# Performance work log

Hardware: AMD Instinct MI355X
Metric: run time of the kernel (lower is better)

The kernel has to match this reference:

```python
import jax, jax.numpy as jnp
import numpy as np

H = 8          # num_heads
D = 32         # out_feats per head
E = 500_000    # number of metapath instances (edges)
N = 100_000    # number of destination nodes
NEG_SLOPE = 0.01


def setup_inputs() -> dict:
    key = jax.random.key(0)
    k1, k2, k3 = jax.random.split(key, 3)
    feat0 = jax.random.normal(k1, (E, H * D), dtype=jnp.float32)
    # learned parameter attn_r [1, H, D] (xavier_normal in torch; plain normal suffices)
    attn_r = jax.random.normal(k2, (1, H, D), dtype=jnp.float32) * 0.1
    dst_idx = jax.random.randint(k3, (E,), 0, N)
    return {"feat0": feat0, "attn_r": attn_r, "dst_idx": dst_idx, "num_dst": N}


def reference(feat0, attn_r, dst_idx, num_dst):
    # [E, H, D] per-head metapath-instance features (feat_drop is identity in eval)
    h = feat0.reshape(-1, H, D)
    # er = sum(h * attn_r) over feature dim -> [E, H]
    er = jnp.sum(h * attn_r, axis=-1)
    # leaky relu on edge scores
    e = jnp.where(er > 0, er, NEG_SLOPE * er)
    # per-destination-node edge softmax (stable: subtract segment max)
    emax = jax.lax.stop_gradient(
        jax.ops.segment_max(e, dst_idx, num_segments=num_dst))  # [N, H]
    num = jnp.exp(e - emax[dst_idx])                            # [E, H]
    den = jax.ops.segment_sum(num, dst_idx, num_segments=num_dst)  # [N, H]
    a = num / den[dst_idx]                                      # [E, H]
    # attention-weighted scatter-sum aggregation: sum_e a_e * h_e per dst node
    m = h * a[..., None]                                        # [E, H, D]
    out = jax.ops.segment_sum(m, dst_idx, num_segments=num_dst)  # [N, H, D]
    # ELU activation then flatten heads
    out = jnp.where(out > 0, out, jnp.expm1(out))
    return out.reshape(num_dst, H * D)
```

## Files before the change

kernel.cpp:

```cpp
#include <hip/hip_runtime.h>
#include <hip/hip_bf16.h>

#define H 8
#define D 32
#define HD 256
#define NEG_SLOPE 0.01f

typedef float f32x4 __attribute__((ext_vector_type(4)));


__global__ void hist_kernel(const int* __restrict__ dst, int E, int* __restrict__ count) {
    int i = blockIdx.x * blockDim.x + threadIdx.x;
    int base = i * 4;
    if (base + 3 < E) {
        int4 d = *reinterpret_cast<const int4*>(dst + base);
        atomicAdd(&count[d.x], 1);
        atomicAdd(&count[d.y], 1);
        atomicAdd(&count[d.z], 1);
        atomicAdd(&count[d.w], 1);
    } else {
        for (int k = base; k < E; ++k) atomicAdd(&count[dst[k]], 1);
    }
}

__global__ void scan_block_kernel(const int* __restrict__ in, int n,
                                  int* __restrict__ out_excl, int* __restrict__ bsum) {
    __shared__ int s[256];
    int t = threadIdx.x;
    int i = blockIdx.x * 256 + t;
    int v = (i < n) ? in[i] : 0;
    s[t] = v;
    __syncthreads();
    for (int off = 1; off < 256; off <<= 1) {
        int x = (t >= off) ? s[t - off] : 0;
        __syncthreads();
        s[t] += x;
        __syncthreads();
    }
    if (i < n) out_excl[i] = s[t] - v;
    if (t == 255) bsum[blockIdx.x] = s[255];
}

__global__ void scan_single_kernel(int* __restrict__ data, int n) {
    __shared__ int s[1024];
    int t = threadIdx.x;
    int v = (t < n) ? data[t] : 0;
    s[t] = v;
    __syncthreads();
    for (int off = 1; off < 1024; off <<= 1) {
        int x = (t >= off) ? s[t - off] : 0;
        __syncthreads();
        s[t] += x;
        __syncthreads();
    }
    if (t < n) data[t] = s[t] - v;
}

__global__ void add_base_kernel(int* __restrict__ off, const int* __restrict__ bsum,
                                int n, int* __restrict__ cursor) {
    int i = blockIdx.x * blockDim.x + threadIdx.x;
    if (i < n) {
        int o = off[i] + bsum[i >> 8];
        off[i] = o;
        cursor[i] = o;
    }
}

__global__ void scatter_kernel(const int* __restrict__ dst, int E,
                               int* __restrict__ cursor, int* __restrict__ csr) {
    int i = blockIdx.x * blockDim.x + threadIdx.x;
    int base = i * 4;
    if (base + 3 < E) {
        int4 d = *reinterpret_cast<const int4*>(dst + base);
        int p0 = atomicAdd(&cursor[d.x], 1); csr[p0] = base;
        int p1 = atomicAdd(&cursor[d.y], 1); csr[p1] = base + 1;
        int p2 = atomicAdd(&cursor[d.z], 1); csr[p2] = base + 2;
        int p3 = atomicAdd(&cursor[d.w], 1); csr[p3] = base + 3;
    } else {
        for (int k = base; k < E; ++k) {
            int p = atomicAdd(&cursor[dst[k]], 1);
            csr[p] = k;
        }
    }
}

__global__ void aggregate_kernel(const float* __restrict__ feat,
                                 const float* __restrict__ attn_r,
                                 const int* __restrict__ csr,
                                 const int* __restrict__ offsets,
                                 const int* __restrict__ count,
                                 float* __restrict__ out, int N) {
    int gtid = blockIdx.x * blockDim.x + threadIdx.x;
    int node = gtid >> 6;
    int lane = threadIdx.x & 63;
    if (node >= N) return;

    f32x4 ar = reinterpret_cast<const f32x4*>(attn_r)[lane];
    int start = offsets[node];
    int len   = count[node];

    f32x4 acc = (f32x4)(0.f);
    float den = 0.f;

    const f32x4* featv = reinterpret_cast<const f32x4*>(feat);

    for (int base = 0; base < len; base += 64) {
        int rem = min(64, len - base);
        int iclamp = min(lane, rem - 1);
        int eidx   = csr[start + base + iclamp];

        int e0 = __shfl(eidx, 0);
        f32x4 f0 = __builtin_nontemporal_load(&featv[(size_t)e0 * 64 + lane]);
        f32x4 f1 = f0, f2 = f0, f3 = f0;
        if (rem > 1) { int e = __shfl(eidx, 1); f1 = __builtin_nontemporal_load(&featv[(size_t)e * 64 + lane]); }
        if (rem > 2) { int e = __shfl(eidx, 2); f2 = __builtin_nontemporal_load(&featv[(size_t)e * 64 + lane]); }
        if (rem > 3) { int e = __shfl(eidx, 3); f3 = __builtin_nontemporal_load(&featv[(size_t)e * 64 + lane]); }

        for (int k = 0; k < rem; ++k) {
            f32x4 f = f0;
            f0 = f1; f1 = f2; f2 = f3;
            int kn = k + 4;
            if (kn < rem) {
                int en = __shfl(eidx, kn);
                f3 = __builtin_nontemporal_load(&featv[(size_t)en * 64 + lane]);
            }
            float part = f.x * ar.x + f.y * ar.y + f.z * ar.z + f.w * ar.w;
            part += __shfl_xor(part, 1);
            part += __shfl_xor(part, 2);
            part += __shfl_xor(part, 4);
            float er  = part;
            float el  = (er > 0.f) ? er : NEG_SLOPE * er;
            float num = __expf(el);
            den   += num;
            acc.x += num * f.x;
            acc.y += num * f.y;
            acc.z += num * f.z;
            acc.w += num * f.w;
        }
    }

    float inv = (len > 0) ? (1.0f / den) : 0.0f;
    f32x4 o;
    o.x = acc.x * inv;
    o.y = acc.y * inv;
    o.z = acc.z * inv;
    o.w = acc.w * inv;
    o.x = (o.x > 0.f) ? o.x : expm1f(o.x);
    o.y = (o.y > 0.f) ? o.y : expm1f(o.y);
    o.z = (o.z > 0.f) ? o.z : expm1f(o.z);
    o.w = (o.w > 0.f) ? o.w : expm1f(o.w);
    __builtin_nontemporal_store(o, &reinterpret_cast<f32x4*>(out)[(size_t)node * 64 + lane]);
}


extern "C" void kernel_launch(void* const* d_in, const int* in_sizes, int n_in,
                              void* d_out, int out_size, void* d_ws, size_t ws_size,
                              hipStream_t stream) {
    const float* feat   = (const float*)d_in[0];
    const float* attn_r = (const float*)d_in[1];
    const int*   dst    = (const int*)d_in[2];
    float*       out    = (float*)d_out;

    const int E = in_sizes[0] / HD;
    const int N = out_size / HD;
    const int NB = (N + 255) / 256;

    int* count   = (int*)d_ws;
    int* offsets = count + N;
    int* cursor  = offsets + N;
    int* bsum    = cursor + N;
    int* csr     = bsum + 1024;

    (void)hipMemsetAsync(count, 0, (size_t)N * sizeof(int), stream);

    const int E4 = (E + 3) / 4;
    hist_kernel<<<(E4 + 255) / 256, 256, 0, stream>>>(dst, E, count);
    scan_block_kernel<<<NB, 256, 0, stream>>>(count, N, offsets, bsum);
    scan_single_kernel<<<1, 1024, 0, stream>>>(bsum, NB);
    add_base_kernel<<<NB, 256, 0, stream>>>(offsets, bsum, N, cursor);
    scatter_kernel<<<(E4 + 255) / 256, 256, 0, stream>>>(dst, E, cursor, csr);

    aggregate_kernel<<<(N + 3) / 4, 256, 0, stream>>>(feat, attn_r, csr, offsets, count, out, N);
}
```

Measured before the change: 175.6 us.

## Fuse block-sum scan into add_base, pack offsets/counts, batch feature loads by 8

Removes the single-block scan launch by having each add_base block redundantly scan the block sums in shared memory. Offset and count are packed into one int2 array so the aggregate kernel does a single load per node. The per-edge rolling 4-deep prefetch is replaced with batches of 8 independent gathers issued before processing. The aim is fewer launches and more memory-level parallelism on the feature gather, at the cost of more registers and a 512-block limit on the fused scan.

```diff
diff --git a/kernel.cpp b/kernel.cpp
--- a/kernel.cpp
+++ b/kernel.cpp
@@ -41,27 +41,29 @@
     if (t == 255) bsum[blockIdx.x] = s[255];
 }
 
-__global__ void scan_single_kernel(int* __restrict__ data, int n) {
-    __shared__ int s[1024];
+__global__ void add_base_kernel(const int* __restrict__ off_excl,
+                                const int* __restrict__ count,
+                                const int* __restrict__ bsum, int nb, int n,
+                                int2* __restrict__ pack, int* __restrict__ cursor) {
+    __shared__ int s[512];
     int t = threadIdx.x;
-    int v = (t < n) ? data[t] : 0;
-    s[t] = v;
+    s[t] = (t < nb) ? bsum[t] : 0;
+    s[t + 256] = (t + 256 < nb) ? bsum[t + 256] : 0;
     __syncthreads();
-    for (int off = 1; off < 1024; off <<= 1) {
-        int x = (t >= off) ? s[t - off] : 0;
+    for (int off = 1; off < 512; off <<= 1) {
+        int x0 = (t >= off) ? s[t - off] : 0;
+        int x1 = (t + 256 >= off) ? s[t + 256 - off] : 0;
         __syncthreads();
-        s[t] += x;
+        s[t] += x0;
+        s[t + 256] += x1;
         __syncthreads();
     }
-    if (t < n) data[t] = s[t] - v;
-}
-
-__global__ void add_base_kernel(int* __restrict__ off, const int* __restrict__ bsum,
-                                int n, int* __restrict__ cursor) {
-    int i = blockIdx.x * blockDim.x + threadIdx.x;
+    int b = blockIdx.x;
+    int base = (b > 0) ? s[b - 1] : 0;
+    int i = b * 256 + t;
     if (i < n) {
-        int o = off[i] + bsum[i >> 8];
-        off[i] = o;
+        int o = off_excl[i] + base;
+        pack[i] = make_int2(o, count[i]);
         cursor[i] = o;
     }
 }
@@ -87,8 +89,7 @@
 __global__ void aggregate_kernel(const float* __restrict__ feat,
                                  const float* __restrict__ attn_r,
                                  const int* __restrict__ csr,
-                                 const int* __restrict__ offsets,
-                                 const int* __restrict__ count,
+                                 const int2* __restrict__ pack,
                                  float* __restrict__ out, int N) {
     int gtid = blockIdx.x * blockDim.x + threadIdx.x;
     int node = gtid >> 6;
@@ -96,48 +97,50 @@
     if (node >= N) return;
 
     f32x4 ar = reinterpret_cast<const f32x4*>(attn_r)[lane];
-    int start = offsets[node];
-    int len   = count[node];
+    int2 se  = pack[node];
+    int start = se.x;
+    int len   = se.y;
 
     f32x4 acc = (f32x4)(0.f);
     float den = 0.f;
 
     const f32x4* featv = reinterpret_cast<const f32x4*>(feat);
 
+#define LOADF(i, fi) if (r > (i)) { int e = __shfl(eidx, c + (i)); \
+    fi = __builtin_nontemporal_load(&featv[(size_t)e * 64 + lane]); }
+#define PROC(fi) { \
+    float part = fi.x * ar.x + fi.y * ar.y + fi.z * ar.z + fi.w * ar.w; \
+    part += __shfl_xor(part, 1); \
+    part += __shfl_xor(part, 2); \
+    part += __shfl_xor(part, 4); \
+    float el  = (part > 0.f) ? part : NEG_SLOPE * part; \
+    float num = __expf(el); \
+    den   += num; \
+    acc.x += num * fi.x; acc.y += num * fi.y; \
+    acc.z += num * fi.z; acc.w += num * fi.w; }
+
     for (int base = 0; base < len; base += 64) {
         int rem = min(64, len - base);
-        int iclamp = min(lane, rem - 1);
-        int eidx   = csr[start + base + iclamp];
+        int eidx = csr[start + base + min(lane, rem - 1)];
 
-        int e0 = __shfl(eidx, 0);
-        f32x4 f0 = __builtin_nontemporal_load(&featv[(size_t)e0 * 64 + lane]);
-        f32x4 f1 = f0, f2 = f0, f3 = f0;
-        if (rem > 1) { int e = __shfl(eidx, 1); f1 = __builtin_nontemporal_load(&featv[(size_t)e * 64 + lane]); }
-        if (rem > 2) { int e = __shfl(eidx, 2); f2 = __builtin_nontemporal_load(&featv[(size_t)e * 64 + lane]); }
-        if (rem > 3) { int e = __shfl(eidx, 3); f3 = __builtin_nontemporal_load(&featv[(size_t)e * 64 + lane]); }
-
-        for (int k = 0; k < rem; ++k) {
-            f32x4 f = f0;
-            f0 = f1; f1 = f2; f2 = f3;
-            int kn = k + 4;
-            if (kn < rem) {
-                int en = __shfl(eidx, kn);
-                f3 = __builtin_nontemporal_load(&featv[(size_t)en * 64 + lane]);
-            }
-            float part = f.x * ar.x + f.y * ar.y + f.z * ar.z + f.w * ar.w;
-            part += __shfl_xor(part, 1);
-            part += __shfl_xor(part, 2);
-            part += __shfl_xor(part, 4);
-            float er  = part;
-            float el  = (er > 0.f) ? er : NEG_SLOPE * er;
-            float num = __expf(el);
-            den   += num;
-            acc.x += num * f.x;
-            acc.y += num * f.y;
-            acc.z += num * f.z;
-            acc.w += num * f.w;
+        for (int c = 0; c < rem; c += 8) {
+            int r = rem - c;
+            f32x4 f0, f1, f2, f3, f4, f5, f6, f7;
+            { int e = __shfl(eidx, c); f0 = __builtin_nontemporal_load(&featv[(size_t)e * 64 + lane]); }
+            LOADF(1, f1) LOADF(2, f2) LOADF(3, f3)
+            LOADF(4, f4) LOADF(5, f5) LOADF(6, f6) LOADF(7, f7)
+            PROC(f0)
+            if (r > 1) PROC(f1)
+            if (r > 2) PROC(f2)
+            if (r > 3) PROC(f3)
+            if (r > 4) PROC(f4)
+            if (r > 5) PROC(f5)
+            if (r > 6) PROC(f6)
+            if (r > 7) PROC(f7)
         }
     }
+#undef LOADF
+#undef PROC
 
     float inv = (len > 0) ? (1.0f / den) : 0.0f;
     f32x4 o;
@@ -165,20 +168,20 @@
     const int N = out_size / HD;
     const int NB = (N + 255) / 256;
 
-    int* count   = (int*)d_ws;
-    int* offsets = count + N;
-    int* cursor  = offsets + N;
-    int* bsum    = cursor + N;
-    int* csr     = bsum + 1024;
+    int*  count    = (int*)d_ws;
+    int*  off_excl = count + N;
+    int*  cursor   = off_excl + N;
+    int*  bsum     = cursor + N;
+    int2* pack     = (int2*)(bsum + 512);
+    int*  csr      = (int*)(pack + N);
 
     (void)hipMemsetAsync(count, 0, (size_t)N * sizeof(int), stream);
 
     const int E4 = (E + 3) / 4;
     hist_kernel<<<(E4 + 255) / 256, 256, 0, stream>>>(dst, E, count);
-    scan_block_kernel<<<NB, 256, 0, stream>>>(count, N, offsets, bsum);
-    scan_single_kernel<<<1, 1024, 0, stream>>>(bsum, NB);
-    add_base_kernel<<<NB, 256, 0, stream>>>(offsets, bsum, N, cursor);
+    scan_block_kernel<<<NB, 256, 0, stream>>>(count, N, off_excl, bsum);
+    add_base_kernel<<<NB, 256, 0, stream>>>(off_excl, count, bsum, NB, N, pack, cursor);
     scatter_kernel<<<(E4 + 255) / 256, 256, 0, stream>>>(dst, E, cursor, csr);
 
-    aggregate_kernel<<<(N + 3) / 4, 256, 0, stream>>>(feat, attn_r, csr, offsets, count, out, N);
+    aggregate_kernel<<<(N + 3) / 4, 256, 0, stream>>>(feat, attn_r, csr, pack, out, N);
 }
```

Result: faster. 170.3 us (-3.0%).
